# Kernel tuning notes

Hardware: AMD Instinct MI355X
Metric: run time of the kernel (lower is better)

The kernel has to match this reference:

```python
import jax, jax.numpy as jnp
import numpy as np

B, S, D, H, F, L = 8, 1024, 512, 8, 2048, 2
SLOTS, OUT = 512, 32
NEG = jnp.finfo(jnp.float32).min


def _ln(x, scale, bias, eps=1e-6):
    mu = jnp.mean(x, axis=-1, keepdims=True)
    var = jnp.var(x, axis=-1, keepdims=True)
    return (x - mu) * jax.lax.rsqrt(var + eps) * scale + bias


def _mha(q_in, kv_in, Wq, Wk, Wv, Wo, mask):
    # flax MultiHeadDotProductAttention, use_bias=False; query scaled by 1/sqrt(head_dim)
    hd = D // H
    b = q_in.shape[0]
    q = (q_in @ Wq).reshape(b, -1, H, hd) / jnp.sqrt(jnp.float32(hd))
    k = (kv_in @ Wk).reshape(b, -1, H, hd)
    v = (kv_in @ Wv).reshape(b, -1, H, hd)
    scores = jnp.einsum('bqhd,bkhd->bhqk', q, k)
    scores = jnp.where(mask, scores, NEG)
    w = jax.nn.softmax(scores, axis=-1)
    o = jnp.einsum('bhqk,bkhd->bqhd', w, v).reshape(b, -1, D)
    return o @ Wo


def _forward(s, x, t, Wq, Wk, Wv, Wo, cWq, cWk, cWv, cWo, ln1_s, ln1_b, ln2_s, ln2_b, ln3_s, ln3_b, W1, b1, W2, b2, lnf_s, lnf_b, Wout, bout, W_vs, b_vs, W_ss, b_ss):
    causal = jnp.tril(jnp.ones((S, S), dtype=bool))[None, None]  # [1,1,S,S]
    eye = jnp.eye(S, dtype=bool)[None, None]                     # [1,1,S,S]
    dec = s
    for l in range(L):
        dec = _ln(dec + _mha(dec, dec, Wq[l], Wk[l], Wv[l], Wo[l], causal), ln1_s[l], ln1_b[l])
        dec = _ln(dec + _mha(dec, t, cWq[l], cWk[l], cWv[l], cWo[l], eye), ln2_s[l], ln2_b[l])
        ff = jax.nn.relu(dec @ W1[l] + b1[l]) @ W2[l] + b2[l]
        dec = _ln(dec + ff, ln3_s[l], ln3_b[l])
    logits = _ln(dec, lnf_s, lnf_b) @ Wout + bout  # [B,S,D]
    keys = jax.nn.softmax(logits.reshape(-1, logits.shape[-1]), axis=1)  # [N,D]
    Vs = (keys @ W_vs + b_vs).reshape(-1, SLOTS, OUT)  # [N,slots,out]
    Ss = keys @ W_ss + b_ss                            # [N,slots]
    xf = x.reshape(-1, OUT)                            # [N,out]
    denom = jnp.linalg.norm(Vs, axis=2) * jnp.linalg.norm(xf, axis=1, keepdims=True)  # [N,slots]
    scores = jnp.einsum('nko,no->nk', Vs, xf) / denom
    idx = jnp.argmax(scores, axis=1)  # [N]
    s_out = jnp.take_along_axis(Ss, idx[:, None], axis=1).reshape(-1, S)            # [B,S]
    v_out = jnp.take_along_axis(Vs, idx[:, None, None], axis=1).reshape(-1, S, OUT)  # [B,S,out]
    return v_out, s_out, Ss


def setup_inputs():
    key = jax.random.key(0)
    ks = iter(jax.random.split(key, 32))
    def r(shape, sc=0.02):
        return jax.random.normal(next(ks), shape, jnp.float32) * sc
    return {
        's': jax.random.normal(next(ks), (B, S, D), jnp.float32),
        'x': jax.random.normal(next(ks), (B, S, OUT), jnp.float32),
        't': jax.random.normal(next(ks), (B, S, D), jnp.float32),
        'Wq': r((L, D, D)), 'Wk': r((L, D, D)), 'Wv': r((L, D, D)), 'Wo': r((L, D, D)),
        'cWq': r((L, D, D)), 'cWk': r((L, D, D)), 'cWv': r((L, D, D)), 'cWo': r((L, D, D)),
        'ln1_s': jnp.ones((L, D)), 'ln1_b': jnp.zeros((L, D)),
        'ln2_s': jnp.ones((L, D)), 'ln2_b': jnp.zeros((L, D)),
        'ln3_s': jnp.ones((L, D)), 'ln3_b': jnp.zeros((L, D)),
        'W1': r((L, D, F)), 'b1': jnp.zeros((L, F)),
        'W2': r((L, F, D)), 'b2': jnp.zeros((L, D)),
        'lnf_s': jnp.ones((D,)), 'lnf_b': jnp.zeros((D,)),
        'Wout': r((D, D)), 'bout': jnp.zeros((D,)),
        'W_vs': r((D, SLOTS * OUT)), 'b_vs': jnp.zeros((SLOTS * OUT,)),
        'W_ss': r((D, SLOTS)), 'b_ss': jnp.zeros((SLOTS,)),
    }


def reference(s, x, t, Wq, Wk, Wv, Wo, cWq, cWk, cWv, cWo, ln1_s, ln1_b, ln2_s, ln2_b, ln3_s, ln3_b, W1, b1, W2, b2, lnf_s, lnf_b, Wout, bout, W_vs, b_vs, W_ss, b_ss):
    return _forward(s, x, t, Wq, Wk, Wv, Wo, cWq, cWk, cWv, cWo, ln1_s, ln1_b, ln2_s, ln2_b, ln3_s, ln3_b, W1, b1, W2, b2, lnf_s, lnf_b, Wout, bout, W_vs, b_vs, W_ss, b_ss)
```

## Files before the change

### kernel.cpp

```cpp
#include <hip/hip_runtime.h>
#include <math.h>

namespace {
constexpr int kD   = 512;
constexpr int kN   = 8192;
constexpr int kS   = 1024;
constexpr int kHD  = 64;
constexpr int kFF  = 2048;
constexpr int kSL  = 512;
constexpr int kOUT = 32;
}

typedef __bf16 bf16x8 __attribute__((ext_vector_type(8)));
typedef float  f32x4  __attribute__((ext_vector_type(4)));

__device__ inline unsigned short f2bf(float x) {
    unsigned u = __float_as_uint(x);
    return (unsigned short)((u + 0x7FFF + ((u >> 16) & 1)) >> 16);
}
__device__ inline void split2(float x, unsigned short& h, unsigned short& l) {
    unsigned u = __float_as_uint(x);
    unsigned hb = (u + 0x7FFF + ((u >> 16) & 1)) >> 16;
    h = (unsigned short)hb;
    float hf = __uint_as_float(hb << 16);
    l = f2bf(x - hf);
}

template<int MODE, int RELU, int HAS_BIAS>
__global__ __launch_bounds__(512, 2)
void mgemm256_k(const unsigned short* __restrict__ Ah, const unsigned short* __restrict__ Al,
                const unsigned short* __restrict__ Bh, const unsigned short* __restrict__ Bl,
                const float* __restrict__ bias, float* __restrict__ C,
                unsigned short* __restrict__ Ch, unsigned short* __restrict__ Cl,
                const float* __restrict__ X, const float* __restrict__ XN,
                float* __restrict__ SC,
                int M, int N, int K, float alpha)
{
    __shared__ uint4 smem4[8192];
    unsigned char* smem = (unsigned char*)smem4;
    const int tid = threadIdx.x, lane = tid & 63, w = tid >> 6;

    const int gx = gridDim.x;
    int bid = blockIdx.y * gx + blockIdx.x;
    const int nwg = gx * gridDim.y;
    bid = (bid & 7) * (nwg >> 3) + (bid >> 3);
    const int bx = bid % gx, by = bid / gx;
    const int brow = by * 256, bcol = bx * 256;
    const int wr = (w >> 2) * 128, wc = (w & 3) * 64;
    const size_t K2 = (size_t)K * 2;

    const int p = w >> 1, hf = w & 1;
    const unsigned short* SP = (p == 0) ? Ah : (p == 1) ? Al : (p == 2) ? Bh : Bl;
    const int rbase = (p < 2) ? brow : bcol;
    const int cch = ((lane & 3) - ((lane >> 3) & 3)) & 3;
    const unsigned char* src0 = (const unsigned char*)SP
        + (size_t)(rbase + hf * 128 + (lane >> 2)) * K2 + (cch << 4);
    const int ldsw0 = (p << 14) + (hf << 13);

    const int lm = lane & 15, lg = lane >> 4;
    const int sw = ((lg + (lm >> 1)) & 3) << 4;
    const int aoff = (wr + lm) * 64 + sw;
    const int boff = 32768 + (wc + lm) * 64 + sw;

    f32x4 acc[8][4];
#pragma unroll
    for (int i = 0; i < 8; ++i)
#pragma unroll
        for (int j = 0; j < 4; ++j) acc[i][j] = (f32x4)(0.f);

    auto stage = [&](int bufo_, int t_) {
        const unsigned char* s_ = src0 + (size_t)t_ * 64;
#pragma unroll
        for (int j = 0; j < 8; ++j)
            __builtin_amdgcn_global_load_lds(
                (const __attribute__((address_space(1))) unsigned int*)(s_ + (size_t)j * 16 * K2),
                (__attribute__((address_space(3))) unsigned int*)(smem + bufo_ + ldsw0 + j * 1024),
                16, 0, 0);
    };

    const int nt = K >> 5;
    stage(0, 0);
    for (int t = 0; t < nt; ++t) {
        if (t + 1 < nt) {
            stage(((t + 1) & 1) << 16, t + 1);
            asm volatile("s_waitcnt vmcnt(8)" ::: "memory");
        } else {
            asm volatile("s_waitcnt vmcnt(0)" ::: "memory");
        }
        __builtin_amdgcn_s_barrier();
        __builtin_amdgcn_sched_barrier(0);
        const unsigned char* base = smem + ((t & 1) << 16);
        bf16x8 bh[4], bl[4];
#pragma unroll
        for (int n = 0; n < 4; ++n) {
            bh[n] = *(const bf16x8*)(base + boff + n * 1024);
            bl[n] = *(const bf16x8*)(base + boff + 16384 + n * 1024);
        }
#pragma unroll
        for (int m = 0; m < 8; ++m) {
            bf16x8 ah = *(const bf16x8*)(base + aoff + m * 1024);
            bf16x8 al = *(const bf16x8*)(base + aoff + 16384 + m * 1024);
#pragma unroll
            for (int n = 0; n < 4; ++n) {
                acc[m][n] = __builtin_amdgcn_mfma_f32_16x16x32_bf16(al, bh[n], acc[m][n], 0, 0, 0);
                acc[m][n] = __builtin_amdgcn_mfma_f32_16x16x32_bf16(ah, bl[n], acc[m][n], 0, 0, 0);
                acc[m][n] = __builtin_amdgcn_mfma_f32_16x16x32_bf16(ah, bh[n], acc[m][n], 0, 0, 0);
            }
        }
        __builtin_amdgcn_sched_barrier(0);
        __builtin_amdgcn_s_barrier();
    }

    if (MODE == 0 || MODE == 1) {
#pragma unroll
        for (int n = 0; n < 4; ++n) {
            const int colg = bcol + wc + n * 16 + lm;
            const float bv = HAS_BIAS ? bias[colg] : 0.f;
#pragma unroll
            for (int m = 0; m < 8; ++m) {
                const int rowb = brow + wr + m * 16 + lg * 4;
#pragma unroll
                for (int r = 0; r < 4; ++r) {
                    float v = alpha * acc[m][n][r] + bv;
                    if (RELU) v = fmaxf(v, 0.f);
                    if (MODE == 0) {
                        C[(size_t)(rowb + r) * N + colg] = v;
                    } else {
                        unsigned short h, l;
                        split2(v, h, l);
                        Ch[(size_t)(rowb + r) * N + colg] = h;
                        Cl[(size_t)(rowb + r) * N + colg] = l;
                    }
                }
            }
        }
    } else {
        float bv[4];
#pragma unroll
        for (int n = 0; n < 4; ++n) bv[n] = bias[bcol + wc + n * 16 + lm];
        const int slot0 = (bcol + wc) >> 5;
#pragma unroll
        for (int m = 0; m < 8; ++m) {
#pragma unroll
            for (int r = 0; r < 4; ++r) {
                const int row = brow + wr + m * 16 + lg * 4 + r;
                const float x0 = X[(size_t)row * kOUT + lm];
                const float x1 = X[(size_t)row * kOUT + 16 + lm];
                const float xn = XN[row];
#pragma unroll
                for (int s = 0; s < 2; ++s) {
                    const float v0 = acc[m][2 * s][r]     + bv[2 * s];
                    const float v1 = acc[m][2 * s + 1][r] + bv[2 * s + 1];
                    float pd = v0 * x0 + v1 * x1;
                    float pn = v0 * v0 + v1 * v1;
                    pd += __shfl_xor(pd, 1); pd += __shfl_xor(pd, 2);
                    pd += __shfl_xor(pd, 4); pd += __shfl_xor(pd, 8);
                    pn += __shfl_xor(pn, 1); pn += __shfl_xor(pn, 2);
                    pn += __shfl_xor(pn, 4); pn += __shfl_xor(pn, 8);
                    if (lm == 0)
                        SC[(size_t)row * kSL + slot0 + s] = pd / (sqrtf(pn) * xn);
                }
            }
        }
    }
}

template<int MODE, int RELU, int HAS_BIAS>
__global__ __launch_bounds__(256)
void mgemm_k(const unsigned short* __restrict__ Ah, const unsigned short* __restrict__ Al,
             const unsigned short* __restrict__ Bh, const unsigned short* __restrict__ Bl,
             const float* __restrict__ bias, float* __restrict__ C,
             unsigned short* __restrict__ Ch, unsigned short* __restrict__ Cl,
             int M, int N, int K, float alpha)
{
    __shared__ uint4 smem_u4[4096];
    unsigned char* smem = (unsigned char*)smem_u4;
    const int tid  = threadIdx.x;
    const int lane = tid & 63;
    const int w    = tid >> 6;
    const int gx = gridDim.x;
    int bid = blockIdx.y * gx + blockIdx.x;
    const int nwg = gx * gridDim.y;
    bid = (bid & 7) * (nwg >> 3) + (bid >> 3);
    const int bxs = bid % gx, bys = bid / gx;
    const int brow = bys * 128;
    const int bcol = bxs * 128;
    const int wr = (w >> 1) * 64, wc = (w & 1) * 64;
    const size_t Kb = (size_t)K * 2;

    const unsigned short* srcM; int rb;
    if      (w == 0) { srcM = Ah; rb = brow; }
    else if (w == 1) { srcM = Al; rb = brow; }
    else if (w == 2) { srcM = Bh; rb = bcol; }
    else             { srcM = Bl; rb = bcol; }
    const int swzsrc = (((lane & 7) << 4) ^ (((lane >> 3) & 7) << 4));
    const unsigned char* srow = (const unsigned char*)srcM
                              + (size_t)(rb + (lane >> 3)) * Kb + swzsrc;
    unsigned char* dbase = smem + w * 16384;

    const int lm = lane & 15;
    const int lg = lane >> 4;
    const int lswz = (lane & 7);

    f32x4 acc[4][4];
#pragma unroll
    for (int i = 0; i < 4; ++i)
#pragma unroll
        for (int j = 0; j < 4; ++j) acc[i][j] = (f32x4)(0.f);

    for (int k0 = 0; k0 < K; k0 += 64) {
#pragma unroll
        for (int j = 0; j < 16; ++j) {
            const unsigned char* sp = srow + (size_t)(j * 8) * Kb + (size_t)k0 * 2;
            __builtin_amdgcn_global_load_lds(
                (const __attribute__((address_space(1))) unsigned int*)sp,
                (__attribute__((address_space(3))) unsigned int*)(dbase + j * 1024),
                16, 0, 0);
        }
        __syncthreads();
#pragma unroll
        for (int ks = 0; ks < 2; ++ks) {
            const int kf = (((ks << 2) + lg) ^ lswz) << 4;
            bf16x8 bh[4], bl[4];
#pragma unroll
            for (int n = 0; n < 4; ++n) {
                const int r = wc + n * 16 + lm;
                bh[n] = *(const bf16x8*)(smem + 32768 + r * 128 + kf);
                bl[n] = *(const bf16x8*)(smem + 49152 + r * 128 + kf);
            }
#pragma unroll
            for (int m = 0; m < 4; ++m) {
                const int r = wr + m * 16 + lm;
                bf16x8 ah = *(const bf16x8*)(smem +         r * 128 + kf);
                bf16x8 al = *(const bf16x8*)(smem + 16384 + r * 128 + kf);
#pragma unroll
                for (int n = 0; n < 4; ++n) {
                    acc[m][n] = __builtin_amdgcn_mfma_f32_16x16x32_bf16(al, bh[n], acc[m][n], 0, 0, 0);
                    acc[m][n] = __builtin_amdgcn_mfma_f32_16x16x32_bf16(ah, bl[n], acc[m][n], 0, 0, 0);
                    acc[m][n] = __builtin_amdgcn_mfma_f32_16x16x32_bf16(ah, bh[n], acc[m][n], 0, 0, 0);
                }
            }
        }
        __syncthreads();
    }

#pragma unroll
    for (int n = 0; n < 4; ++n) {
        const int colg = bcol + wc + n * 16 + lm;
        const float bv = HAS_BIAS ? bias[colg] : 0.f;
#pragma unroll
        for (int m = 0; m < 4; ++m) {
            const int rowb = brow + wr + m * 16 + lg * 4;
#pragma unroll
            for (int r = 0; r < 4; ++r) {
                float v = alpha * acc[m][n][r] + bv;
                if (RELU) v = fmaxf(v, 0.f);
                if (MODE == 0) {
                    C[(size_t)(rowb + r) * N + colg] = v;
                } else {
                    unsigned short h, l;
                    split2(v, h, l);
                    Ch[(size_t)(rowb + r) * N + colg] = h;
                    Cl[(size_t)(rowb + r) * N + colg] = l;
                }
            }
        }
    }
}

__global__ __launch_bounds__(256)
void tsplit_k(const float* __restrict__ W, unsigned short* __restrict__ TH,
              unsigned short* __restrict__ TL, int K, int N)
{
    __shared__ float t[32][33];
    const int tid = threadIdx.x;
    const int n0 = blockIdx.x * 32, k0 = blockIdx.y * 32;
    {
        const int r = tid >> 3, c = (tid & 7) * 4;
        const float4 v = *(const float4*)(W + (size_t)(k0 + r) * N + n0 + c);
        t[r][c] = v.x; t[r][c + 1] = v.y; t[r][c + 2] = v.z; t[r][c + 3] = v.w;
    }
    __syncthreads();
    const int rn = tid >> 3, ck = (tid & 7) * 4;
    unsigned short h[4], l[4];
#pragma unroll
    for (int i = 0; i < 4; ++i) split2(t[ck + i][rn], h[i], l[i]);
    *(ushort4*)(TH + (size_t)(n0 + rn) * K + k0 + ck) = make_ushort4(h[0], h[1], h[2], h[3]);
    *(ushort4*)(TL + (size_t)(n0 + rn) * K + k0 + ck) = make_ushort4(l[0], l[1], l[2], l[3]);
}

__global__ __launch_bounds__(256)
void split_k(const float* __restrict__ in, unsigned short* __restrict__ hi,
             unsigned short* __restrict__ lo, int n4)
{
    int i = blockIdx.x * 256 + threadIdx.x;
    const int stride = gridDim.x * 256;
    for (; i < n4; i += stride) {
        const float4 v = *(const float4*)(in + (size_t)i * 4);
        unsigned short h[4], l[4];
        split2(v.x, h[0], l[0]); split2(v.y, h[1], l[1]);
        split2(v.z, h[2], l[2]); split2(v.w, h[3], l[3]);
        *(ushort4*)(hi + (size_t)i * 4) = make_ushort4(h[0], h[1], h[2], h[3]);
        *(ushort4*)(lo + (size_t)i * 4) = make_ushort4(l[0], l[1], l[2], l[3]);
    }
}

__global__ __launch_bounds__(256)
void attn_k(const float* __restrict__ Q, const float* __restrict__ K,
            const float* __restrict__ V, float* __restrict__ O)
{
    __shared__ float Qs[64][68];
    __shared__ float Ks[64][68];
    __shared__ float Vs[64][68];
    __shared__ float Ps[64][68];
    const int tid = threadIdx.x;
    const int tr = tid >> 4, tc = tid & 15;
    const int qt = blockIdx.x & 15;
    const int h  = (blockIdx.x >> 4) & 7;
    const int b  = blockIdx.x >> 7;
    const int q0 = qt * 64;
    const float* Qb = Q + ((size_t)(b * kS + q0)) * kD + h * kHD;
    {
        const int r = tid >> 2;
#pragma unroll
        for (int it = 0; it < 4; ++it) {
            const int e0 = ((tid & 3) << 2) + it * 16;
            const float4 q4 = *(const float4*)(Qb + (size_t)r * kD + e0);
            Qs[e0 + 0][r] = q4.x; Qs[e0 + 1][r] = q4.y;
            Qs[e0 + 2][r] = q4.z; Qs[e0 + 3][r] = q4.w;
        }
    }
    float m[4], l[4], acc[4][4];
#pragma unroll
    for (int i = 0; i < 4; ++i) {
        m[i] = -INFINITY; l[i] = 0.f;
#pragma unroll
        for (int j = 0; j < 4; ++j) acc[i][j] = 0.f;
    }
    for (int j0 = 0; j0 <= q0; j0 += 64) {
        const float* Kb = K + ((size_t)(b * kS + j0)) * kD + h * kHD;
        const float* Vb = V + ((size_t)(b * kS + j0)) * kD + h * kHD;
        __syncthreads();
        {
            const int c = tid >> 2;
#pragma unroll
            for (int it = 0; it < 4; ++it) {
                const int e0 = ((tid & 3) << 2) + it * 16;
                const float4 k4 = *(const float4*)(Kb + (size_t)c * kD + e0);
                Ks[e0 + 0][c] = k4.x; Ks[e0 + 1][c] = k4.y;
                Ks[e0 + 2][c] = k4.z; Ks[e0 + 3][c] = k4.w;
                *(float4*)&Vs[c][e0] = *(const float4*)(Vb + (size_t)c * kD + e0);
            }
        }
        __syncthreads();
        float s[4][4];
#pragma unroll
        for (int i = 0; i < 4; ++i)
#pragma unroll
            for (int j = 0; j < 4; ++j) s[i][j] = 0.f;
        for (int e = 0; e < 64; ++e) {
            float qa[4], kb[4];
            *(float4*)&qa[0] = *(const float4*)&Qs[e][tr * 4];
            *(float4*)&kb[0] = *(const float4*)&Ks[e][tc * 4];
#pragma unroll
            for (int i = 0; i < 4; ++i)
#pragma unroll
                for (int j = 0; j < 4; ++j)
                    s[i][j] = fmaf(qa[i], kb[j], s[i][j]);
        }
        if (j0 == q0) {
#pragma unroll
            for (int i = 0; i < 4; ++i)
#pragma unroll
                for (int j = 0; j < 4; ++j)
                    if (tc * 4 + j > tr * 4 + i) s[i][j] = -INFINITY;
        }
#pragma unroll
        for (int i = 0; i < 4; ++i) {
            float rm = fmaxf(fmaxf(s[i][0], s[i][1]), fmaxf(s[i][2], s[i][3]));
            rm = fmaxf(rm, __shfl_xor(rm, 1));
            rm = fmaxf(rm, __shfl_xor(rm, 2));
            rm = fmaxf(rm, __shfl_xor(rm, 4));
            rm = fmaxf(rm, __shfl_xor(rm, 8));
            const float mn = fmaxf(m[i], rm);
            const float co = expf(m[i] - mn);
            float ps = 0.f;
#pragma unroll
            for (int j = 0; j < 4; ++j) { s[i][j] = expf(s[i][j] - mn); ps += s[i][j]; }
            ps += __shfl_xor(ps, 1); ps += __shfl_xor(ps, 2);
            ps += __shfl_xor(ps, 4); ps += __shfl_xor(ps, 8);
            l[i] = l[i] * co + ps;
            m[i] = mn;
#pragma unroll
            for (int j = 0; j < 4; ++j) acc[i][j] *= co;
            *(float4*)&Ps[tr * 4 + i][tc * 4] = make_float4(s[i][0], s[i][1], s[i][2], s[i][3]);
        }
        __syncthreads();
        for (int c = 0; c < 64; ++c) {
            const float4 v4 = *(const float4*)&Vs[c][tc * 4];
#pragma unroll
            for (int i = 0; i < 4; ++i) {
                const float p = Ps[tr * 4 + i][c];
                acc[i][0] = fmaf(p, v4.x, acc[i][0]);
                acc[i][1] = fmaf(p, v4.y, acc[i][1]);
                acc[i][2] = fmaf(p, v4.z, acc[i][2]);
                acc[i][3] = fmaf(p, v4.w, acc[i][3]);
            }
        }
    }
    float* Ob = O + ((size_t)(b * kS + q0)) * kD + h * kHD;
#pragma unroll
    for (int i = 0; i < 4; ++i) {
        const float inv = 1.0f / l[i];
        *(float4*)(Ob + (size_t)(tr * 4 + i) * kD + tc * 4) =
            make_float4(acc[i][0] * inv, acc[i][1] * inv, acc[i][2] * inv, acc[i][3] * inv);
    }
}

__global__ __launch_bounds__(256)
void ln_k(const float* __restrict__ a, const float* __restrict__ b,
          const float* __restrict__ sc, const float* __restrict__ bi,
          float* __restrict__ out, unsigned short* __restrict__ oh,
          unsigned short* __restrict__ ol)
{
    const int w = threadIdx.x >> 6, lane = threadIdx.x & 63;
    const size_t row = (size_t)blockIdx.x * 4 + w;
    const float* ap = a + row * kD;
    float x[8];
    *(float4*)&x[0] = *(const float4*)(ap + lane * 8);
    *(float4*)&x[4] = *(const float4*)(ap + lane * 8 + 4);
    if (b) {
        const float* bp = b + row * kD;
        float y[8];
        *(float4*)&y[0] = *(const float4*)(bp + lane * 8);
        *(float4*)&y[4] = *(const float4*)(bp + lane * 8 + 4);
#pragma unroll
        for (int k = 0; k < 8; ++k) x[k] += y[k];
    }
    float s = 0.f;
#pragma unroll
    for (int k = 0; k < 8; ++k) s += x[k];
    for (int msk = 1; msk < 64; msk <<= 1) s += __shfl_xor(s, msk);
    const float mean = s * (1.0f / 512.0f);
    float v = 0.f;
#pragma unroll
    for (int k = 0; k < 8; ++k) { const float d = x[k] - mean; v = fmaf(d, d, v); }
    for (int msk = 1; msk < 64; msk <<= 1) v += __shfl_xor(v, msk);
    const float rstd = 1.0f / sqrtf(v * (1.0f / 512.0f) + 1e-6f);
    float o[8]; unsigned short h[8], lo2[8];
#pragma unroll
    for (int k = 0; k < 8; ++k) {
        const int col = lane * 8 + k;
        o[k] = (x[k] - mean) * rstd * sc[col] + bi[col];
        split2(o[k], h[k], lo2[k]);
    }
    *(float4*)(out + row * kD + lane * 8)     = *(const float4*)&o[0];
    *(float4*)(out + row * kD + lane * 8 + 4) = *(const float4*)&o[4];
    *(ushort4*)(oh + row * kD + lane * 8)     = make_ushort4(h[0], h[1], h[2], h[3]);
    *(ushort4*)(oh + row * kD + lane * 8 + 4) = make_ushort4(h[4], h[5], h[6], h[7]);
    *(ushort4*)(ol + row * kD + lane * 8)     = make_ushort4(lo2[0], lo2[1], lo2[2], lo2[3]);
    *(ushort4*)(ol + row * kD + lane * 8 + 4) = make_ushort4(lo2[4], lo2[5], lo2[6], lo2[7]);
}

__global__ __launch_bounds__(256)
void softmax_k(const float* __restrict__ in, float* __restrict__ out,
               unsigned short* __restrict__ oh, unsigned short* __restrict__ ol)
{
    const int w = threadIdx.x >> 6, lane = threadIdx.x & 63;
    const size_t row = (size_t)blockIdx.x * 4 + w;
    const float* ip = in + row * kD;
    float x[8];
    *(float4*)&x[0] = *(const float4*)(ip + lane * 8);
    *(float4*)&x[4] = *(const float4*)(ip + lane * 8 + 4);
    float mx = x[0];
#pragma unroll
    for (int k = 1; k < 8; ++k) mx = fmaxf(mx, x[k]);
    for (int msk = 1; msk < 64; msk <<= 1) mx = fmaxf(mx, __shfl_xor(mx, msk));
    float s = 0.f;
#pragma unroll
    for (int k = 0; k < 8; ++k) { x[k] = expf(x[k] - mx); s += x[k]; }
    for (int msk = 1; msk < 64; msk <<= 1) s += __shfl_xor(s, msk);
    const float inv = 1.0f / s;
    unsigned short h[8], lo2[8];
#pragma unroll
    for (int k = 0; k < 8; ++k) { x[k] *= inv; split2(x[k], h[k], lo2[k]); }
    *(float4*)(out + row * kD + lane * 8)     = *(const float4*)&x[0];
    *(float4*)(out + row * kD + lane * 8 + 4) = *(const float4*)&x[4];
    *(ushort4*)(oh + row * kD + lane * 8)     = make_ushort4(h[0], h[1], h[2], h[3]);
    *(ushort4*)(oh + row * kD + lane * 8 + 4) = make_ushort4(h[4], h[5], h[6], h[7]);
    *(ushort4*)(ol + row * kD + lane * 8)     = make_ushort4(lo2[0], lo2[1], lo2[2], lo2[3]);
    *(ushort4*)(ol + row * kD + lane * 8 + 4) = make_ushort4(lo2[4], lo2[5], lo2[6], lo2[7]);
}

__global__ __launch_bounds__(256)
void xnorm_k(const float* __restrict__ X, float* __restrict__ XN)
{
    const int tid = threadIdx.x;
    const int row = blockIdx.x * 8 + (tid >> 5);
    const int o = tid & 31;
    const float v = X[(size_t)row * kOUT + o];
    float s = v * v;
    s += __shfl_xor(s, 1); s += __shfl_xor(s, 2); s += __shfl_xor(s, 4);
    s += __shfl_xor(s, 8); s += __shfl_xor(s, 16);
    if (o == 0) XN[row] = sqrtf(s);
}

__global__ __launch_bounds__(256)
void pick_k(const float* __restrict__ scores, const float* __restrict__ keys,
            const float* __restrict__ Wvs, const float* __restrict__ bvs,
            const float* __restrict__ Ss, float* __restrict__ vout,
            float* __restrict__ sout)
{
    const int n = blockIdx.x;
    const int tid = threadIdx.x;
    __shared__ float sv[256];
    __shared__ int   si[256];
    __shared__ float ks[512];
    __shared__ float red[256];
    const float s0 = scores[(size_t)n * kSL + tid];
    const float s1 = scores[(size_t)n * kSL + tid + 256];
    float bs; int bi;
    if (s1 > s0) { bs = s1; bi = tid + 256; } else { bs = s0; bi = tid; }
    sv[tid] = bs; si[tid] = bi;
    ks[tid] = keys[(size_t)n * kD + tid];
    ks[tid + 256] = keys[(size_t)n * kD + tid + 256];
    __syncthreads();
    for (int off = 128; off > 0; off >>= 1) {
        if (tid < off) {
            const float ov = sv[tid + off]; const int oi = si[tid + off];
            if (ov > sv[tid] || (ov == sv[tid] && oi < si[tid])) { sv[tid] = ov; si[tid] = oi; }
        }
        __syncthreads();
    }
    const int idx = si[0];
    const int o = tid & 31;
    const int seg = tid >> 5;
    const float* Wc = Wvs + (size_t)idx * kOUT + o;
    float part = 0.f;
    for (int d = seg * 64; d < seg * 64 + 64; ++d)
        part = fmaf(ks[d], Wc[(size_t)d * (kSL * kOUT)], part);
    red[tid] = part;
    __syncthreads();
    if (tid < 32) {
        float t = red[tid];
#pragma unroll
        for (int ss = 1; ss < 8; ++ss) t += red[tid + 32 * ss];
        vout[(size_t)n * kOUT + tid] = t + bvs[idx * kOUT + tid];
    }
    if (tid == 0) sout[n] = Ss[(size_t)n * kSL + idx];
}

extern "C" void kernel_launch(void* const* d_in, const int* in_sizes, int n_in,
                              void* d_out, int out_size, void* d_ws, size_t ws_size,
                              hipStream_t stream)
{
    (void)in_sizes; (void)n_in; (void)out_size; (void)ws_size;
    const float* s_in = (const float*)d_in[0];
    const float* x_in = (const float*)d_in[1];
    const float* t_in = (const float*)d_in[2];
    const float* Wq   = (const float*)d_in[3];
    const float* Wk   = (const float*)d_in[4];
    const float* Wv   = (const float*)d_in[5];
    const float* Wo   = (const float*)d_in[6];
    const float* cWv  = (const float*)d_in[9];
    const float* cWo  = (const float*)d_in[10];
    const float* ln1s = (const float*)d_in[11];
    const float* ln1b = (const float*)d_in[12];
    const float* ln2s = (const float*)d_in[13];
    const float* ln2b = (const float*)d_in[14];
    const float* ln3s = (const float*)d_in[15];
    const float* ln3b = (const float*)d_in[16];
    const float* W1   = (const float*)d_in[17];
    const float* b1   = (const float*)d_in[18];
    const float* W2   = (const float*)d_in[19];
    const float* b2   = (const float*)d_in[20];
    const float* lnfs = (const float*)d_in[21];
    const float* lnfb = (const float*)d_in[22];
    const float* Wout = (const float*)d_in[23];
    const float* bout = (const float*)d_in[24];
    const float* Wvs  = (const float*)d_in[25];
    const float* bvs  = (const float*)d_in[26];
    const float* Wss  = (const float*)d_in[27];
    const float* bss  = (const float*)d_in[28];

    float* out_v  = (float*)d_out;
    float* out_s  = out_v + (size_t)kN * kOUT;
    float* out_Ss = out_s + kN;

    unsigned char* w8 = (unsigned char*)d_ws;
    const size_t MD = (size_t)kN * kD;
    float* f_dec = (float*)w8;
    float* f_A   = f_dec + MD;
    float* f_B   = f_A + MD;
    float* f_C   = f_B + MD;
    float* f_xn  = f_C + MD;
    unsigned short* dH = (unsigned short*)(f_xn + kN);
    unsigned short* dL = dH + MD;
    unsigned short* hH = dL + MD;
    unsigned short* hL = hH + (size_t)kN * kFF;
    unsigned short* wTH = hL + (size_t)kN * kFF;
    unsigned short* wTL = wTH + (size_t)kSL * kOUT * kD;
    unsigned short* sH = hH;
    unsigned short* sL = hL;
    unsigned short* kH = hH + MD;
    unsigned short* kL = hL + MD;

    const dim3 blk(256);
    const dim3 blk512(512);
    const size_t DD = (size_t)kD * kD;

    auto tsplit = [&](const float* W, int K, int N) {
        tsplit_k<<<dim3(N / 32, K / 32), blk, 0, stream>>>(W, wTH, wTL, K, N);
    };
    auto gemm = [&](const unsigned short* aH, const unsigned short* aL,
                    const float* bias, float* out, int N, int K, float alpha) {
        if (bias)
            mgemm_k<0, 0, 1><<<dim3(N / 128, kN / 128), blk, 0, stream>>>(
                aH, aL, wTH, wTL, bias, out, nullptr, nullptr, kN, N, K, alpha);
        else
            mgemm_k<0, 0, 0><<<dim3(N / 128, kN / 128), blk, 0, stream>>>(
                aH, aL, wTH, wTL, nullptr, out, nullptr, nullptr, kN, N, K, alpha);
    };

    xnorm_k<<<kN / 8, blk, 0, stream>>>(x_in, f_xn);
    split_k<<<1024, blk, 0, stream>>>(s_in, dH, dL, (int)(MD / 4));

    const float* cur = s_in;
    for (int l = 0; l < 2; ++l) {
        const size_t wo = (size_t)l * DD;
        tsplit(Wq + wo, kD, kD); gemm(dH, dL, nullptr, f_A, kD, kD, 0.125f);
        tsplit(Wk + wo, kD, kD); gemm(dH, dL, nullptr, f_B, kD, kD, 1.f);
        tsplit(Wv + wo, kD, kD); gemm(dH, dL, nullptr, f_C, kD, kD, 1.f);
        attn_k<<<1024, blk, 0, stream>>>(f_A, f_B, f_C, f_A);
        split_k<<<1024, blk, 0, stream>>>(f_A, sH, sL, (int)(MD / 4));
        tsplit(Wo + wo, kD, kD); gemm(sH, sL, nullptr, f_B, kD, kD, 1.f);
        ln_k<<<kN / 4, blk, 0, stream>>>(cur, f_B, ln1s + l * kD, ln1b + l * kD, f_dec, dH, dL);
        split_k<<<1024, blk, 0, stream>>>(t_in, sH, sL, (int)(MD / 4));
        tsplit(cWv + wo, kD, kD); gemm(sH, sL, nullptr, f_A, kD, kD, 1.f);
        split_k<<<1024, blk, 0, stream>>>(f_A, sH, sL, (int)(MD / 4));
        tsplit(cWo + wo, kD, kD); gemm(sH, sL, nullptr, f_A, kD, kD, 1.f);
        ln_k<<<kN / 4, blk, 0, stream>>>(f_dec, f_A, ln2s + l * kD, ln2b + l * kD, f_dec, dH, dL);
        tsplit(W1 + (size_t)l * kD * kFF, kD, kFF);
        mgemm256_k<1, 1, 1><<<dim3(kFF / 256, kN / 256), blk512, 0, stream>>>(
            dH, dL, wTH, wTL, b1 + (size_t)l * kFF, nullptr, hH, hL,
            nullptr, nullptr, nullptr, kN, kFF, kD, 1.f);
        tsplit(W2 + (size_t)l * kFF * kD, kFF, kD);
        gemm(hH, hL, b2 + (size_t)l * kD, f_A, kD, kFF, 1.f);
        ln_k<<<kN / 4, blk, 0, stream>>>(f_dec, f_A, ln3s + l * kD, ln3b + l * kD, f_dec, dH, dL);
        cur = f_dec;
    }
    ln_k<<<kN / 4, blk, 0, stream>>>(f_dec, nullptr, lnfs, lnfb, f_A, dH, dL);
    tsplit(Wout, kD, kD); gemm(dH, dL, bout, f_B, kD, kD, 1.f);
    softmax_k<<<kN / 4, blk, 0, stream>>>(f_B, f_A, kH, kL);
    tsplit(Wss, kD, kSL); gemm(kH, kL, bss, out_Ss, kSL, kD, 1.f);
    tsplit(Wvs, kD, kSL * kOUT);
    mgemm256_k<2, 0, 1><<<dim3(kSL * kOUT / 256, kN / 256), blk512, 0, stream>>>(
        kH, kL, wTH, wTL, bvs, nullptr, nullptr, nullptr, x_in, f_xn, f_C,
        kN, kSL * kOUT, kD, 1.f);
    pick_k<<<kN, blk, 0, stream>>>(f_C, f_A, Wvs, bvs, out_Ss, out_v, out_s);
}
```

Before: 2.119 ms.

## Fuse QKV projection, emit split bf16 from attention, pipeline big GEMM main loop

Concatenates Wq/Wk/Wv into one 1536-wide GEMM, with attention reading the packed QKV buffer and applying the 1/sqrt(hd) scale itself. Attention and the cross-attention V projection now write hi/lo bf16 directly, which removes separate split passes. The 256-tile GEMM main loop is restructured into per-row-block phases that prefetch LDS fragments and issue global-to-LDS loads in halves, adding s_setprio around MFMAs to overlap memory with compute. This cuts kernel launches and memory round-trips, at the cost of more register pressure and more barriers per K step in the big GEMM.

```diff
diff --git a/kernel.cpp b/kernel.cpp
--- a/kernel.cpp
+++ b/kernel.cpp
@@ -9,6 +9,7 @@
 constexpr int kFF  = 2048;
 constexpr int kSL  = 512;
 constexpr int kOUT = 32;
+constexpr int kLQ  = 1536;
 }
 
 typedef __bf16 bf16x8 __attribute__((ext_vector_type(8)));
@@ -36,6 +37,7 @@
                 float* __restrict__ SC,
                 int M, int N, int K, float alpha)
 {
+    (void)M;
     __shared__ uint4 smem4[8192];
     unsigned char* smem = (unsigned char*)smem4;
     const int tid = threadIdx.x, lane = tid & 63, w = tid >> 6;
@@ -49,13 +51,13 @@
     const int wr = (w >> 2) * 128, wc = (w & 3) * 64;
     const size_t K2 = (size_t)K * 2;
 
-    const int p = w >> 1, hf = w & 1;
-    const unsigned short* SP = (p == 0) ? Ah : (p == 1) ? Al : (p == 2) ? Bh : Bl;
-    const int rbase = (p < 2) ? brow : bcol;
+    const int pl = w >> 1, hf = w & 1;
+    const unsigned short* SP = (pl == 0) ? Ah : (pl == 1) ? Al : (pl == 2) ? Bh : Bl;
+    const int rbase = (pl < 2) ? brow : bcol;
     const int cch = ((lane & 3) - ((lane >> 3) & 3)) & 3;
     const unsigned char* src0 = (const unsigned char*)SP
         + (size_t)(rbase + hf * 128 + (lane >> 2)) * K2 + (cch << 4);
-    const int ldsw0 = (p << 14) + (hf << 13);
+    const int ldsw0 = (pl << 14) + (hf << 13);
 
     const int lm = lane & 15, lg = lane >> 4;
     const int sw = ((lg + (lm >> 1)) & 3) << 4;
@@ -68,47 +70,83 @@
 #pragma unroll
         for (int j = 0; j < 4; ++j) acc[i][j] = (f32x4)(0.f);
 
-    auto stage = [&](int bufo_, int t_) {
+    auto stage4 = [&](int bufo_, int t_, int j0_) {
         const unsigned char* s_ = src0 + (size_t)t_ * 64;
 #pragma unroll
-        for (int j = 0; j < 8; ++j)
+        for (int j = 0; j < 4; ++j)
             __builtin_amdgcn_global_load_lds(
-                (const __attribute__((address_space(1))) unsigned int*)(s_ + (size_t)j * 16 * K2),
-                (__attribute__((address_space(3))) unsigned int*)(smem + bufo_ + ldsw0 + j * 1024),
+                (const __attribute__((address_space(1))) unsigned int*)(s_ + (size_t)(j0_ + j) * 16 * K2),
+                (__attribute__((address_space(3))) unsigned int*)(smem + bufo_ + ldsw0 + (j0_ + j) * 1024),
                 16, 0, 0);
     };
 
     const int nt = K >> 5;
-    stage(0, 0);
+    stage4(0, 0, 0); stage4(0, 0, 4);
+    asm volatile("s_waitcnt vmcnt(0)" ::: "memory");
+    __builtin_amdgcn_s_barrier();
+
+    bf16x8 rBh[4], rBl[4], nBh[4], nBl[4], ah_c, al_c, ah_n, al_n;
+#pragma unroll
+    for (int n = 0; n < 4; ++n) {
+        rBh[n] = *(const bf16x8*)(smem + boff + n * 1024);
+        rBl[n] = *(const bf16x8*)(smem + boff + 16384 + n * 1024);
+        nBh[n] = rBh[n]; nBl[n] = rBl[n];
+    }
+    ah_c = *(const bf16x8*)(smem + aoff);
+    al_c = *(const bf16x8*)(smem + aoff + 16384);
+    ah_n = ah_c; al_n = al_c;
+
+#pragma unroll 1
     for (int t = 0; t < nt; ++t) {
-        if (t + 1 < nt) {
-            stage(((t + 1) & 1) << 16, t + 1);
-            asm volatile("s_waitcnt vmcnt(8)" ::: "memory");
-        } else {
-            asm volatile("s_waitcnt vmcnt(0)" ::: "memory");
-        }
-        __builtin_amdgcn_s_barrier();
-        __builtin_amdgcn_sched_barrier(0);
-        const unsigned char* base = smem + ((t & 1) << 16);
-        bf16x8 bh[4], bl[4];
-#pragma unroll
-        for (int n = 0; n < 4; ++n) {
-            bh[n] = *(const bf16x8*)(base + boff + n * 1024);
-            bl[n] = *(const bf16x8*)(base + boff + 16384 + n * 1024);
-        }
-#pragma unroll
-        for (int m = 0; m < 8; ++m) {
-            bf16x8 ah = *(const bf16x8*)(base + aoff + m * 1024);
-            bf16x8 al = *(const bf16x8*)(base + aoff + 16384 + m * 1024);
+        unsigned char* cb = smem + ((t & 1) << 16);
+        unsigned char* nb = smem + (((t + 1) & 1) << 16);
+        const bool nl = (t + 1 < nt);
+#pragma unroll
+        for (int ph = 0; ph < 8; ++ph) {
+            if (ph < 7) {
+                ah_n = *(const bf16x8*)(cb + aoff + (ph + 1) * 1024);
+                al_n = *(const bf16x8*)(cb + aoff + 16384 + (ph + 1) * 1024);
+            }
+            if (nl) {
+                if (ph == 0) stage4(((t + 1) & 1) << 16, t + 1, 0);
+                if (ph == 1) stage4(((t + 1) & 1) << 16, t + 1, 4);
+                if (ph == 6) {
+#pragma unroll
+                    for (int n = 0; n < 2; ++n) {
+                        nBh[n] = *(const bf16x8*)(nb + boff + n * 1024);
+                        nBl[n] = *(const bf16x8*)(nb + boff + 16384 + n * 1024);
+                    }
+                }
+                if (ph == 7) {
+#pragma unroll
+                    for (int n = 2; n < 4; ++n) {
+                        nBh[n] = *(const bf16x8*)(nb + boff + n * 1024);
+                        nBl[n] = *(const bf16x8*)(nb + boff + 16384 + n * 1024);
+                    }
+                    ah_n = *(const bf16x8*)(nb + aoff);
+                    al_n = *(const bf16x8*)(nb + aoff + 16384);
+                }
+            }
+            __builtin_amdgcn_sched_barrier(0);
+            if (ph == 5 && nl) asm volatile("s_waitcnt vmcnt(0)" ::: "memory");
+            __builtin_amdgcn_s_barrier();
+            __builtin_amdgcn_sched_barrier(0);
+            __builtin_amdgcn_s_setprio(1);
 #pragma unroll
             for (int n = 0; n < 4; ++n) {
-                acc[m][n] = __builtin_amdgcn_mfma_f32_16x16x32_bf16(al, bh[n], acc[m][n], 0, 0, 0);
-                acc[m][n] = __builtin_amdgcn_mfma_f32_16x16x32_bf16(ah, bl[n], acc[m][n], 0, 0, 0);
-                acc[m][n] = __builtin_amdgcn_mfma_f32_16x16x32_bf16(ah, bh[n], acc[m][n], 0, 0, 0);
-            }
-        }
-        __builtin_amdgcn_sched_barrier(0);
-        __builtin_amdgcn_s_barrier();
+                acc[ph][n] = __builtin_amdgcn_mfma_f32_16x16x32_bf16(al_c, rBh[n], acc[ph][n], 0, 0, 0);
+                acc[ph][n] = __builtin_amdgcn_mfma_f32_16x16x32_bf16(ah_c, rBl[n], acc[ph][n], 0, 0, 0);
+                acc[ph][n] = __builtin_amdgcn_mfma_f32_16x16x32_bf16(ah_c, rBh[n], acc[ph][n], 0, 0, 0);
+            }
+            __builtin_amdgcn_s_setprio(0);
+            __builtin_amdgcn_sched_barrier(0);
+            __builtin_amdgcn_s_barrier();
+            ah_c = ah_n; al_c = al_n;
+            if (ph == 7 && nl) {
+#pragma unroll
+                for (int n = 0; n < 4; ++n) { rBh[n] = nBh[n]; rBl[n] = nBl[n]; }
+            }
+        }
     }
 
     if (MODE == 0 || MODE == 1) {
@@ -306,8 +344,8 @@
 }
 
 __global__ __launch_bounds__(256)
-void attn_k(const float* __restrict__ Q, const float* __restrict__ K,
-            const float* __restrict__ V, float* __restrict__ O)
+void attn_k(const float* __restrict__ QKV,
+            unsigned short* __restrict__ OH, unsigned short* __restrict__ OL)
 {
     __shared__ float Qs[64][68];
     __shared__ float Ks[64][68];
@@ -319,15 +357,15 @@
     const int h  = (blockIdx.x >> 4) & 7;
     const int b  = blockIdx.x >> 7;
     const int q0 = qt * 64;
-    const float* Qb = Q + ((size_t)(b * kS + q0)) * kD + h * kHD;
+    const float* Qb = QKV + ((size_t)(b * kS + q0)) * kLQ + h * kHD;
     {
         const int r = tid >> 2;
 #pragma unroll
         for (int it = 0; it < 4; ++it) {
             const int e0 = ((tid & 3) << 2) + it * 16;
-            const float4 q4 = *(const float4*)(Qb + (size_t)r * kD + e0);
-            Qs[e0 + 0][r] = q4.x; Qs[e0 + 1][r] = q4.y;
-            Qs[e0 + 2][r] = q4.z; Qs[e0 + 3][r] = q4.w;
+            const float4 q4 = *(const float4*)(Qb + (size_t)r * kLQ + e0);
+            Qs[e0 + 0][r] = q4.x * 0.125f; Qs[e0 + 1][r] = q4.y * 0.125f;
+            Qs[e0 + 2][r] = q4.z * 0.125f; Qs[e0 + 3][r] = q4.w * 0.125f;
         }
     }
     float m[4], l[4], acc[4][4];
@@ -338,18 +376,18 @@
         for (int j = 0; j < 4; ++j) acc[i][j] = 0.f;
     }
     for (int j0 = 0; j0 <= q0; j0 += 64) {
-        const float* Kb = K + ((size_t)(b * kS + j0)) * kD + h * kHD;
-        const float* Vb = V + ((size_t)(b * kS + j0)) * kD + h * kHD;
+        const float* Kb = QKV + ((size_t)(b * kS + j0)) * kLQ + 512 + h * kHD;
+        const float* Vb = QKV + ((size_t)(b * kS + j0)) * kLQ + 1024 + h * kHD;
         __syncthreads();
         {
             const int c = tid >> 2;
 #pragma unroll
             for (int it = 0; it < 4; ++it) {
                 const int e0 = ((tid & 3) << 2) + it * 16;
-                const float4 k4 = *(const float4*)(Kb + (size_t)c * kD + e0);
+                const float4 k4 = *(const float4*)(Kb + (size_t)c * kLQ + e0);
                 Ks[e0 + 0][c] = k4.x; Ks[e0 + 1][c] = k4.y;
                 Ks[e0 + 2][c] = k4.z; Ks[e0 + 3][c] = k4.w;
-                *(float4*)&Vs[c][e0] = *(const float4*)(Vb + (size_t)c * kD + e0);
+                *(float4*)&Vs[c][e0] = *(const float4*)(Vb + (size_t)c * kLQ + e0);
             }
         }
         __syncthreads();
@@ -408,12 +446,16 @@
             }
         }
     }
-    float* Ob = O + ((size_t)(b * kS + q0)) * kD + h * kHD;
+    const size_t ob = ((size_t)(b * kS + q0)) * kD + h * kHD;
 #pragma unroll
     for (int i = 0; i < 4; ++i) {
         const float inv = 1.0f / l[i];
-        *(float4*)(Ob + (size_t)(tr * 4 + i) * kD + tc * 4) =
-            make_float4(acc[i][0] * inv, acc[i][1] * inv, acc[i][2] * inv, acc[i][3] * inv);
+        unsigned short hh[4], ll[4];
+#pragma unroll
+        for (int j = 0; j < 4; ++j) split2(acc[i][j] * inv, hh[j], ll[j]);
+        const size_t off = ob + (size_t)(tr * 4 + i) * kD + tc * 4;
+        *(ushort4*)(OH + off) = make_ushort4(hh[0], hh[1], hh[2], hh[3]);
+        *(ushort4*)(OL + off) = make_ushort4(ll[0], ll[1], ll[2], ll[3]);
     }
 }
 
@@ -600,26 +642,18 @@
     unsigned short* hL = hH + (size_t)kN * kFF;
     unsigned short* wTH = hL + (size_t)kN * kFF;
     unsigned short* wTL = wTH + (size_t)kSL * kOUT * kD;
+    float* f_qkv = f_A;
     unsigned short* sH = hH;
     unsigned short* sL = hL;
-    unsigned short* kH = hH + MD;
-    unsigned short* kL = hL + MD;
+    unsigned short* kH = hH;
+    unsigned short* kL = hL;
 
     const dim3 blk(256);
     const dim3 blk512(512);
     const size_t DD = (size_t)kD * kD;
 
-    auto tsplit = [&](const float* W, int K, int N) {
-        tsplit_k<<<dim3(N / 32, K / 32), blk, 0, stream>>>(W, wTH, wTL, K, N);
-    };
-    auto gemm = [&](const unsigned short* aH, const unsigned short* aL,
-                    const float* bias, float* out, int N, int K, float alpha) {
-        if (bias)
-            mgemm_k<0, 0, 1><<<dim3(N / 128, kN / 128), blk, 0, stream>>>(
-                aH, aL, wTH, wTL, bias, out, nullptr, nullptr, kN, N, K, alpha);
-        else
-            mgemm_k<0, 0, 0><<<dim3(N / 128, kN / 128), blk, 0, stream>>>(
-                aH, aL, wTH, wTL, nullptr, out, nullptr, nullptr, kN, N, K, alpha);
+    auto tsplit = [&](const float* W, int Kd, int Nd, unsigned short* TH, unsigned short* TL) {
+        tsplit_k<<<dim3(Nd / 32, Kd / 32), blk, 0, stream>>>(W, TH, TL, Kd, Nd);
     };
 
     xnorm_k<<<kN / 8, blk, 0, stream>>>(x_in, f_xn);
@@ -628,34 +662,45 @@
     const float* cur = s_in;
     for (int l = 0; l < 2; ++l) {
         const size_t wo = (size_t)l * DD;
-        tsplit(Wq + wo, kD, kD); gemm(dH, dL, nullptr, f_A, kD, kD, 0.125f);
-        tsplit(Wk + wo, kD, kD); gemm(dH, dL, nullptr, f_B, kD, kD, 1.f);
-        tsplit(Wv + wo, kD, kD); gemm(dH, dL, nullptr, f_C, kD, kD, 1.f);
-        attn_k<<<1024, blk, 0, stream>>>(f_A, f_B, f_C, f_A);
-        split_k<<<1024, blk, 0, stream>>>(f_A, sH, sL, (int)(MD / 4));
-        tsplit(Wo + wo, kD, kD); gemm(sH, sL, nullptr, f_B, kD, kD, 1.f);
-        ln_k<<<kN / 4, blk, 0, stream>>>(cur, f_B, ln1s + l * kD, ln1b + l * kD, f_dec, dH, dL);
+        tsplit(Wq + wo, kD, kD, wTH,             wTL);
+        tsplit(Wk + wo, kD, kD, wTH + 512 * kD,  wTL + 512 * kD);
+        tsplit(Wv + wo, kD, kD, wTH + 1024 * kD, wTL + 1024 * kD);
+        mgemm_k<0, 0, 0><<<dim3(kLQ / 128, kN / 128), blk, 0, stream>>>(
+            dH, dL, wTH, wTL, nullptr, f_qkv, nullptr, nullptr, kN, kLQ, kD, 1.f);
+        attn_k<<<1024, blk, 0, stream>>>(f_qkv, sH, sL);
+        tsplit(Wo + wo, kD, kD, wTH, wTL);
+        mgemm_k<0, 0, 0><<<dim3(4, 64), blk, 0, stream>>>(
+            sH, sL, wTH, wTL, nullptr, f_A, nullptr, nullptr, kN, kD, kD, 1.f);
+        ln_k<<<kN / 4, blk, 0, stream>>>(cur, f_A, ln1s + l * kD, ln1b + l * kD, f_dec, dH, dL);
         split_k<<<1024, blk, 0, stream>>>(t_in, sH, sL, (int)(MD / 4));
-        tsplit(cWv + wo, kD, kD); gemm(sH, sL, nullptr, f_A, kD, kD, 1.f);
-        split_k<<<1024, blk, 0, stream>>>(f_A, sH, sL, (int)(MD / 4));
-        tsplit(cWo + wo, kD, kD); gemm(sH, sL, nullptr, f_A, kD, kD, 1.f);
+        tsplit(cWv + wo, kD, kD, wTH, wTL);
+        mgemm_k<1, 0, 0><<<dim3(4, 64), blk, 0, stream>>>(
+            sH, sL, wTH, wTL, nullptr, nullptr, dH, dL, kN, kD, kD, 1.f);
+        tsplit(cWo + wo, kD, kD, wTH, wTL);
+        mgemm_k<0, 0, 0><<<dim3(4, 64), blk, 0, stream>>>(
+            dH, dL, wTH, wTL, nullptr, f_A, nullptr, nullptr, kN, kD, kD, 1.f);
         ln_k<<<kN / 4, blk, 0, stream>>>(f_dec, f_A, ln2s + l * kD, ln2b + l * kD, f_dec, dH, dL);
-        tsplit(W1 + (size_t)l * kD * kFF, kD, kFF);
+        tsplit(W1 + (size_t)l * kD * kFF, kD, kFF, wTH, wTL);
         mgemm256_k<1, 1, 1><<<dim3(kFF / 256, kN / 256), blk512, 0, stream>>>(
             dH, dL, wTH, wTL, b1 + (size_t)l * kFF, nullptr, hH, hL,
             nullptr, nullptr, nullptr, kN, kFF, kD, 1.f);
-        tsplit(W2 + (size_t)l * kFF * kD, kFF, kD);
-        gemm(hH, hL, b2 + (size_t)l * kD, f_A, kD, kFF, 1.f);
+        tsplit(W2 + (size_t)l * kFF * kD, kFF, kD, wTH, wTL);
+        mgemm_k<0, 0, 1><<<dim3(4, 64), blk, 0, stream>>>(
+            hH, hL, wTH, wTL, b2 + (size_t)l * kD, f_A, nullptr, nullptr, kN, kD, kFF, 1.f);
         ln_k<<<kN / 4, blk, 0, stream>>>(f_dec, f_A, ln3s + l * kD, ln3b + l * kD, f_dec, dH, dL);
         cur = f_dec;
     }
     ln_k<<<kN / 4, blk, 0, stream>>>(f_dec, nullptr, lnfs, lnfb, f_A, dH, dL);
-    tsplit(Wout, kD, kD); gemm(dH, dL, bout, f_B, kD, kD, 1.f);
-    softmax_k<<<kN / 4, blk, 0, stream>>>(f_B, f_A, kH, kL);
-    tsplit(Wss, kD, kSL); gemm(kH, kL, bss, out_Ss, kSL, kD, 1.f);
-    tsplit(Wvs, kD, kSL * kOUT);
+    tsplit(Wout, kD, kD, wTH, wTL);
+    mgemm_k<0, 0, 1><<<dim3(4, 64), blk, 0, stream>>>(
+        dH, dL, wTH, wTL, bout, f_B, nullptr, nullptr, kN, kD, kD, 1.f);
+    softmax_k<<<kN / 4, blk, 0, stream>>>(f_B, f_C, kH, kL);
+    tsplit(Wss, kD, kSL, wTH, wTL);
+    mgemm_k<0, 0, 1><<<dim3(4, 64), blk, 0, stream>>>(
+        kH, kL, wTH, wTL, bss, out_Ss, nullptr, nullptr, kN, kSL, kD, 1.f);
+    tsplit(Wvs, kD, kSL * kOUT, wTH, wTL);
     mgemm256_k<2, 0, 1><<<dim3(kSL * kOUT / 256, kN / 256), blk512, 0, stream>>>(
-        kH, kL, wTH, wTL, bvs, nullptr, nullptr, nullptr, x_in, f_xn, f_C,
+        kH, kL, wTH, wTL, bvs, nullptr, nullptr, nullptr, x_in, f_xn, f_B,
         kN, kSL * kOUT, kD, 1.f);
-    pick_k<<<kN, blk, 0, stream>>>(f_C, f_A, Wvs, bvs, out_Ss, out_v, out_s);
-}
+    pick_k<<<kN, blk, 0, stream>>>(f_B, f_C, Wvs, bvs, out_Ss, out_v, out_s);
+}
```

Result: slower. 2.204 ms (+4.0%).
